# Kernel tuning notes

Hardware: AMD Instinct MI355X
Metric: run time of the kernel (lower is better)

## Reference

```python
import jax, jax.numpy as jnp
import numpy as np

B, T, C = 4, 2048, 1024
N_HEAD = 16
D_HEAD = C // N_HEAD


def setup_inputs() -> dict:
    key = jax.random.key(0)
    ks = jax.random.split(key, 5)
    s_in = 1.0 / np.sqrt(C)
    return {
        "x": jax.random.normal(ks[0], (B, T, C), dtype=jnp.float32),
        "Wqkv": jax.random.uniform(ks[1], (C, 3 * C), dtype=jnp.float32, minval=-s_in, maxval=s_in),
        "bqkv": jax.random.uniform(ks[2], (3 * C,), dtype=jnp.float32, minval=-s_in, maxval=s_in),
        "Wproj": jax.random.uniform(ks[3], (C, C), dtype=jnp.float32, minval=-s_in, maxval=s_in),
        "bproj": jax.random.uniform(ks[4], (C,), dtype=jnp.float32, minval=-s_in, maxval=s_in),
    }


def reference(x, Wqkv, bqkv, Wproj, bproj):
    b, t, c = x.shape
    qkv = x @ Wqkv + bqkv                      # [B,T,3C]
    q, k, v = jnp.split(qkv, 3, axis=2)
    # [B,T,H,Dh] -> [B,H,T,Dh]
    q = q.reshape(b, t, N_HEAD, D_HEAD).transpose(0, 2, 1, 3)
    k = k.reshape(b, t, N_HEAD, D_HEAD).transpose(0, 2, 1, 3)
    v = v.reshape(b, t, N_HEAD, D_HEAD).transpose(0, 2, 1, 3)
    scale = 1.0 / np.sqrt(D_HEAD).astype(np.float32)
    att = jnp.einsum("bhqd,bhkd->bhqk", q, k) * scale   # [B,H,T,T]
    causal = jnp.tril(jnp.ones((t, t), dtype=bool))
    att = jnp.where(causal, att, jnp.float32(-jnp.inf))
    att = jax.nn.softmax(att, axis=-1)
    y = jnp.einsum("bhqk,bhkd->bhqd", att, v)            # [B,H,T,Dh]
    y = y.transpose(0, 2, 1, 3).reshape(b, t, c)
    return y @ Wproj + bproj
```

## Files before the change

kernel.cpp:

```cpp
#include <hip/hip_runtime.h>

using u16 = unsigned short;
typedef __attribute__((ext_vector_type(8))) __bf16 bf16x8;
typedef __attribute__((ext_vector_type(4))) float f32x4;
typedef __attribute__((ext_vector_type(16))) float f32x16;
typedef __attribute__((ext_vector_type(4))) unsigned int u32x4;
typedef __attribute__((ext_vector_type(2))) unsigned int u32x2;

__device__ inline u16 f2bf(float f) {
    unsigned u = __float_as_uint(f);
    u += 0x7FFFu + ((u >> 16) & 1u);
    return (u16)(u >> 16);
}
__device__ inline unsigned pack2(float a, float b) {
    return (unsigned)f2bf(a) | ((unsigned)f2bf(b) << 16);
}
__device__ inline bf16x8 as_bf16x8(u32x4 v) {
    union { u32x4 u; bf16x8 b; } x; x.u = v; return x.b;
}
__device__ inline unsigned cvtpk(float lo, float hi) {
    unsigned w;
    asm("v_cvt_pk_bf16_f32 %0, %1, %2" : "=v"(w) : "v"(lo), "v"(hi));
    return w;
}
__device__ inline void gload_lds16(const void* g, void* l) {
    __builtin_amdgcn_global_load_lds(
        (const __attribute__((address_space(1))) void*)g,
        (__attribute__((address_space(3))) void*)l, 16, 0, 0);
}
__device__ inline void ring_barrier() {
    __builtin_amdgcn_sched_barrier(0);
    asm volatile("s_waitcnt lgkmcnt(0)" ::: "memory");
    __builtin_amdgcn_sched_barrier(0);
    __builtin_amdgcn_s_barrier();
    __builtin_amdgcn_sched_barrier(0);
}

__global__ __launch_bounds__(256) void xcast(const float* __restrict__ in,
                                             u16* __restrict__ out) {
    const size_t i = ((size_t)blockIdx.x * 256 + threadIdx.x) * 8;
    f32x4 a = *(const f32x4*)(in + i);
    f32x4 b = *(const f32x4*)(in + i + 4);
    u32x4 w;
    w[0] = pack2(a[0], a[1]); w[1] = pack2(a[2], a[3]);
    w[2] = pack2(b[0], b[1]); w[3] = pack2(b[2], b[3]);
    *(u32x4*)(out + i) = w;
}

__global__ __launch_bounds__(256) void tcast2(const float* __restrict__ Wqkv,
                                              const float* __restrict__ Wproj,
                                              u16* __restrict__ Wtq,
                                              u16* __restrict__ Wtp) {
    __shared__ float tile[64][65];
    const int by = blockIdx.y;
    const float* in;
    u16* out;
    int C, c0;
    if (by < 48) { in = Wqkv;  out = Wtq; C = 3072; c0 = by * 64; }
    else         { in = Wproj; out = Wtp; C = 1024; c0 = (by - 48) * 64; }
    const int R = 1024, r0 = blockIdx.x * 64;
    const int t = threadIdx.x;
    {
        const int r = t >> 2, cq = (t & 3) * 16;
        const float* src = in + (size_t)(r0 + r) * C + c0 + cq;
#pragma unroll
        for (int j = 0; j < 4; ++j) {
            f32x4 v = *(const f32x4*)(src + j * 4);
#pragma unroll
            for (int e = 0; e < 4; ++e) tile[r][cq + j * 4 + e] = v[e];
        }
    }
    __syncthreads();
    {
        const int c = t >> 2, rq = (t & 3) * 16;
        u32x4 w0, w1;
#pragma unroll
        for (int j = 0; j < 4; ++j) {
            w0[j] = pack2(tile[rq + 2 * j][c], tile[rq + 2 * j + 1][c]);
            w1[j] = pack2(tile[rq + 8 + 2 * j][c], tile[rq + 8 + 2 * j + 1][c]);
        }
        u16* dst = out + (size_t)(c0 + c) * R + r0 + rq;
        *(u32x4*)dst = w0;
        *(u32x4*)(dst + 8) = w1;
    }
}

template <int EPI>
__global__ __launch_bounds__(256) void gemm_kernel(const u16* __restrict__ A,
                                                   const u16* __restrict__ Bt,
                                                   const float* __restrict__ bias,
                                                   void* __restrict__ outp,
                                                   u16* __restrict__ vtp,
                                                   const int M, const int N, const int K) {
    __shared__ char lds[49152];
    const int t = threadIdx.x;
    const int l = t & 63, wid = t >> 6;
    const int wr = wid >> 1, wc = wid & 1;
    const int g = l >> 4, lr = l & 15;
    const int m0 = blockIdx.x * 128, n0 = blockIdx.y * 128;

    f32x4 acc[4][4];
#pragma unroll
    for (int i = 0; i < 4; ++i)
#pragma unroll
        for (int j = 0; j < 4; ++j)
#pragma unroll
            for (int e = 0; e < 4; ++e) acc[i][j][e] = 0.f;

    const size_t Kb2 = (size_t)K * 2;
    const size_t rowbA = (size_t)(m0 + wid * 16 + (l >> 2)) * Kb2 + (l & 3) * 16;
    const size_t rowbB = (size_t)(n0 + wid * 16 + (l >> 2)) * Kb2 + (l & 3) * 16;
    const int kn = K >> 5;

    auto STAGE = [&](int kk) {
        char* buf = lds + (kk % 3) * 16384;
        const size_t kb = (size_t)kk * 64;
#pragma unroll
        for (int j = 0; j < 2; ++j) {
            gload_lds16((const char*)A + rowbA + j * 64 * Kb2 + kb,
                        buf + j * 4096 + wid * 1024);
            gload_lds16((const char*)Bt + rowbB + j * 64 * Kb2 + kb,
                        buf + 8192 + j * 4096 + wid * 1024);
        }
    };

    STAGE(0); STAGE(1);
#pragma unroll 1
    for (int kk = 0; kk < kn; ++kk) {
        if (kk + 1 < kn) asm volatile("s_waitcnt vmcnt(4)" ::: "memory");
        else             asm volatile("s_waitcnt vmcnt(0)" ::: "memory");
        ring_barrier();
        if (kk + 2 < kn) STAGE(kk + 2);
        const char* As = lds + (kk % 3) * 16384;
        const char* Bs = As + 8192;
        bf16x8 a[4], b[4];
#pragma unroll
        for (int m = 0; m < 4; ++m) {
            const int row = wr * 64 + m * 16 + lr;
            a[m] = as_bf16x8(*(const u32x4*)(As + row * 64 + g * 16));
        }
#pragma unroll
        for (int n = 0; n < 4; ++n) {
            const int row = wc * 64 + n * 16 + lr;
            b[n] = as_bf16x8(*(const u32x4*)(Bs + row * 64 + g * 16));
        }
        __builtin_amdgcn_s_setprio(1);
#pragma unroll
        for (int m = 0; m < 4; ++m)
#pragma unroll
            for (int n = 0; n < 4; ++n)
                acc[m][n] = __builtin_amdgcn_mfma_f32_16x16x32_bf16(a[m], b[n], acc[m][n], 0, 0, 0);
        __builtin_amdgcn_s_setprio(0);
    }

    const float qsc = (EPI == 0 && n0 < 1024) ? 0.18033688f : 1.0f;
#pragma unroll
    for (int m = 0; m < 4; ++m) {
#pragma unroll
        for (int n = 0; n < 4; ++n) {
            const int colg = n0 + wc * 64 + n * 16 + lr;
            const float bv = bias[colg];
            if constexpr (EPI == 0) {
                const int sec = colg >> 10, c = colg & 1023;
                const int hh = c >> 6, dd = c & 63;
                if (sec == 2) {
                    const int rowg0 = m0 + wr * 64 + m * 16 + g * 4;
                    const int bb = rowg0 >> 11, tt = rowg0 & 2047;
                    u16 pk[4];
#pragma unroll
                    for (int r = 0; r < 4; ++r)
                        pk[r] = f2bf(acc[m][n][r] + bv);
                    u16* dst = vtp + (((size_t)(bb * 16 + hh) * 64 + dd) << 11) + tt;
                    unsigned w0 = (unsigned)pk[0] | ((unsigned)pk[1] << 16);
                    unsigned w1 = (unsigned)pk[2] | ((unsigned)pk[3] << 16);
                    u32x2 wv; wv[0] = w0; wv[1] = w1;
                    *(u32x2*)dst = wv;
                } else {
#pragma unroll
                    for (int r = 0; r < 4; ++r) {
                        const int rowg = m0 + wr * 64 + m * 16 + g * 4 + r;
                        const float v = (acc[m][n][r] + bv) * qsc;
                        const int bb = rowg >> 11, tt = rowg & 2047;
                        u16* dst = (u16*)outp;
                        dst[(size_t)sec * 8388608u +
                            (((size_t)(bb * 16 + hh) * 2048 + tt) << 6) + dd] = f2bf(v);
                    }
                }
            } else {
#pragma unroll
                for (int r = 0; r < 4; ++r) {
                    const int rowg = m0 + wr * 64 + m * 16 + g * 4 + r;
                    ((float*)outp)[(size_t)rowg * N + colg] = acc[m][n][r] + bv;
                }
            }
        }
    }
}

__global__ __launch_bounds__(256) void attn_kernel(const u16* __restrict__ Q,
                                                   const u16* __restrict__ K,
                                                   const u16* __restrict__ Vt,
                                                   u16* __restrict__ Y) {
    __shared__ char lds[32768];
    const int t = threadIdx.x;
    const int l = t & 63, w = t >> 6;
    const int q = l & 31, hi = l >> 5;
    const int id = (int)blockIdx.y * 16 + (int)blockIdx.x;
    const int p = 15 - (id >> 6);
    const int bh = id & 63;
    const char* Kby = (const char*)(K + (size_t)bh * 131072);
    const char* Vby = (const char*)(Vt + (size_t)bh * 131072);
    const u16* Qb = Q + (size_t)bh * 131072;
    const int bb = bh >> 4, hh = bh & 15;
    const unsigned ck = (unsigned)(((l & 7) ^ (l >> 3)) << 4);
    const unsigned rd_swz = (unsigned)((q & 7) << 4);

    const int q0w = p * 128 + w * 32;
    const int qg = q0w + q;
    const int NT = 2 * p + 2;
    const int ntw = ((q0w + 31) >> 6) + 1;

    bf16x8 qf[4];
#pragma unroll
    for (int ks = 0; ks < 4; ++ks)
        qf[ks] = as_bf16x8(*(const u32x4*)(Qb + (size_t)(q0w + q) * 64 + ks * 16 + hi * 8));

    f32x16 o0, o1;
#pragma unroll
    for (int r = 0; r < 16; ++r) { o0[r] = 0.f; o1[r] = 0.f; }
    float lacc = 0.f;

    auto STAGE = [&](int it) {
        const int kv0 = it << 6;
        char* base = lds + (it & 1) * 16384;
#pragma unroll
        for (int j = 0; j < 2; ++j) {
            const int r = w * 16 + j * 8 + (l >> 3);
            gload_lds16(Kby + (size_t)(kv0 + r) * 128 + ck,
                        base + w * 2048 + j * 1024);
            gload_lds16(Vby + (size_t)r * 4096 + (size_t)kv0 * 2 + ck,
                        base + 8192 + w * 2048 + j * 1024);
        }
    };

    STAGE(0);
#pragma unroll 1
    for (int it = 0; it < NT; ++it) {
        asm volatile("s_waitcnt vmcnt(0)" ::: "memory");
        ring_barrier();
        if (it + 1 < NT) STAGE(it + 1);
        if (it < ntw) {
            const int kv0 = it << 6;
            const char* Kl = lds + (it & 1) * 16384;
            const char* Vl = Kl + 8192;
            u32x4 vf[8];
#pragma unroll
            for (int kvb = 0; kvb < 2; ++kvb)
#pragma unroll
                for (int s = 0; s < 2; ++s)
#pragma unroll
                    for (int db = 0; db < 2; ++db)
                        vf[kvb * 4 + s * 2 + db] = *(const u32x4*)(
                            Vl + (unsigned)((db * 32 + q) * 128) +
                            ((unsigned)(kvb * 64 + s * 32 + hi * 16) ^ rd_swz));
            f32x16 s0, s1;
#pragma unroll
            for (int r = 0; r < 16; ++r) { s0[r] = 0.f; s1[r] = 0.f; }
            __builtin_amdgcn_s_setprio(1);
#pragma unroll
            for (int ks = 0; ks < 4; ++ks) {
                const unsigned co = (unsigned)(ks * 32 + hi * 16) ^ rd_swz;
                bf16x8 kf0 = as_bf16x8(*(const u32x4*)(Kl + (unsigned)(q * 128) + co));
                s0 = __builtin_amdgcn_mfma_f32_32x32x16_bf16(kf0, qf[ks], s0, 0, 0, 0);
                bf16x8 kf1 = as_bf16x8(*(const u32x4*)(Kl + (unsigned)((32 + q) * 128) + co));
                s1 = __builtin_amdgcn_mfma_f32_32x32x16_bf16(kf1, qf[ks], s1, 0, 0, 0);
            }
            __builtin_amdgcn_s_setprio(0);
            if (kv0 + 63 > q0w) {
#pragma unroll
                for (int r = 0; r < 16; ++r) {
                    const int roff = (r & 3) + 8 * (r >> 2) + hi * 4;
                    if (kv0 + roff > qg) s0[r] = -1.0e30f;
                    if (kv0 + 32 + roff > qg) s1[r] = -1.0e30f;
                }
            }
            float sm[8];
#pragma unroll
            for (int j = 0; j < 8; ++j) {
                s0[2 * j]     = exp2f(s0[2 * j]);
                s0[2 * j + 1] = exp2f(s0[2 * j + 1]);
                s1[2 * j]     = exp2f(s1[2 * j]);
                s1[2 * j + 1] = exp2f(s1[2 * j + 1]);
                sm[j] = (s0[2 * j] + s0[2 * j + 1]) + (s1[2 * j] + s1[2 * j + 1]);
            }
            lacc += ((sm[0] + sm[1]) + (sm[2] + sm[3])) +
                    ((sm[4] + sm[5]) + (sm[6] + sm[7]));
#pragma unroll
            for (int kvb = 0; kvb < 2; ++kvb) {
                unsigned wd[8];
#pragma unroll
                for (int j = 0; j < 8; ++j) {
                    const float plo = kvb ? s1[2 * j] : s0[2 * j];
                    const float phi = kvb ? s1[2 * j + 1] : s0[2 * j + 1];
                    wd[j] = cvtpk(plo, phi);
                }
                u32x2 r0 = __builtin_amdgcn_permlane32_swap(wd[0], wd[2], false, false);
                u32x2 r1 = __builtin_amdgcn_permlane32_swap(wd[1], wd[3], false, false);
                u32x2 r2 = __builtin_amdgcn_permlane32_swap(wd[4], wd[6], false, false);
                u32x2 r3 = __builtin_amdgcn_permlane32_swap(wd[5], wd[7], false, false);
                u32x4 fa, fb;
                fa[0] = r0[0]; fa[1] = r1[0]; fa[2] = r0[1]; fa[3] = r1[1];
                fb[0] = r2[0]; fb[1] = r3[0]; fb[2] = r2[1]; fb[3] = r3[1];
                const bf16x8 pa = as_bf16x8(fa), pb = as_bf16x8(fb);
                __builtin_amdgcn_s_setprio(1);
                o0 = __builtin_amdgcn_mfma_f32_32x32x16_bf16(pa, as_bf16x8(vf[kvb * 4 + 0]), o0, 0, 0, 0);
                o1 = __builtin_amdgcn_mfma_f32_32x32x16_bf16(pa, as_bf16x8(vf[kvb * 4 + 1]), o1, 0, 0, 0);
                o0 = __builtin_amdgcn_mfma_f32_32x32x16_bf16(pb, as_bf16x8(vf[kvb * 4 + 2]), o0, 0, 0, 0);
                o1 = __builtin_amdgcn_mfma_f32_32x32x16_bf16(pb, as_bf16x8(vf[kvb * 4 + 3]), o1, 0, 0, 0);
                __builtin_amdgcn_s_setprio(0);
            }
        }
    }
    float lsum;
    {
        u32x2 rr = __builtin_amdgcn_permlane32_swap(
            __float_as_uint(lacc), __float_as_uint(lacc), false, false);
        lsum = lacc + __uint_as_float(hi ? rr[0] : rr[1]);
    }
    const float linv = 1.f / lsum;
#pragma unroll
    for (int r = 0; r < 16; ++r) {
        const int roff = (r & 3) + 8 * (r >> 2) + hi * 4;
        const float invq = __shfl(linv, roff);
        const size_t base = ((size_t)(bb * 2048 + q0w + roff)) * 1024 + hh * 64 + q;
        Y[base] = f2bf(o0[r] * invq);
        Y[base + 32] = f2bf(o1[r] * invq);
    }
}

extern "C" void kernel_launch(void* const* d_in, const int* in_sizes, int n_in,
                              void* d_out, int out_size, void* d_ws, size_t ws_size,
                              hipStream_t stream) {
    const float* x = (const float*)d_in[0];
    const float* Wqkv = (const float*)d_in[1];
    const float* bqkv = (const float*)d_in[2];
    const float* Wproj = (const float*)d_in[3];
    const float* bproj = (const float*)d_in[4];
    float* out = (float*)d_out;
    char* ws = (char*)d_ws;

    u16* Wtq = (u16*)(ws + 0);
    u16* Wtp = (u16*)(ws + 6291456);
    u16* Qb  = (u16*)(ws + 8388608);
    u16* Yb  = (u16*)(ws + 41943040);
    u16* Vtb = (u16*)(ws + 58720256);
    u16* Xb  = (u16*)(ws + 75497472);

    xcast<<<4096, 256, 0, stream>>>(x, Xb);
    tcast2<<<dim3(16, 64), 256, 0, stream>>>(Wqkv, Wproj, Wtq, Wtp);
    gemm_kernel<0><<<dim3(64, 24), 256, 0, stream>>>(
        Xb, Wtq, bqkv, (void*)Qb, Vtb, 8192, 3072, 1024);
    attn_kernel<<<dim3(16, 64), 256, 0, stream>>>(
        Qb, Qb + 8388608, Vtb, Yb);
    gemm_kernel<1><<<dim3(64, 8), 256, 0, stream>>>(
        Yb, Wtp, bproj, (void*)out, nullptr, 8192, 1024, 1024);
}
```

Baseline: 182.9 us.

## Split longest causal attention query blocks across two workgroups and merge partials

```diff
diff --git a/kernel.cpp b/kernel.cpp
--- a/kernel.cpp
+++ b/kernel.cpp
@@ -197,17 +197,28 @@
     }
 }
 
+static const unsigned char TPj[20] = {11,10, 9, 7,15,15, 8,14,13,13,12,14, 5, 4,12, 6, 0, 2, 1, 3};
+static const unsigned char TCj[20] = { 0, 0, 0, 0, 0, 1, 0, 0, 0, 1, 0, 1, 0, 0, 1, 0, 0, 0, 0, 0};
+static const unsigned char TSj[20] = { 0, 0, 0, 0, 1, 1, 0, 1, 1, 1, 1, 1, 0, 0, 1, 0, 0, 0, 0, 0};
+
 __global__ __launch_bounds__(256) void attn_kernel(const u16* __restrict__ Q,
                                                    const u16* __restrict__ K,
                                                    const u16* __restrict__ Vt,
-                                                   u16* __restrict__ Y) {
+                                                   u16* __restrict__ Y,
+                                                   float* __restrict__ PartO,
+                                                   float* __restrict__ PartL) {
     __shared__ char lds[32768];
     const int t = threadIdx.x;
     const int l = t & 63, w = t >> 6;
     const int q = l & 31, hi = l >> 5;
-    const int id = (int)blockIdx.y * 16 + (int)blockIdx.x;
-    const int p = 15 - (id >> 6);
-    const int bh = id & 63;
+    const int bh = (int)blockIdx.x;
+    const int j = (int)blockIdx.y;
+    const int p  = (int)TPj[j];
+    const int cc = (int)TCj[j];
+    const int sp = (int)TSj[j];
+    const int half = p + 1;
+    const int t0  = (sp && cc) ? half : 0;
+    const int NTc = sp ? half : (2 * p + 2);
     const char* Kby = (const char*)(K + (size_t)bh * 131072);
     const char* Vby = (const char*)(Vt + (size_t)bh * 131072);
     const u16* Qb = Q + (size_t)bh * 131072;
@@ -217,7 +228,6 @@
 
     const int q0w = p * 128 + w * 32;
     const int qg = q0w + q;
-    const int NT = 2 * p + 2;
     const int ntw = ((q0w + 31) >> 6) + 1;
 
     bf16x8 qf[4];
@@ -230,28 +240,29 @@
     for (int r = 0; r < 16; ++r) { o0[r] = 0.f; o1[r] = 0.f; }
     float lacc = 0.f;
 
-    auto STAGE = [&](int it) {
-        const int kv0 = it << 6;
-        char* base = lds + (it & 1) * 16384;
-#pragma unroll
-        for (int j = 0; j < 2; ++j) {
-            const int r = w * 16 + j * 8 + (l >> 3);
+    auto STAGE = [&](int itl) {
+        const int kv0 = (t0 + itl) << 6;
+        char* base = lds + (itl & 1) * 16384;
+#pragma unroll
+        for (int jj = 0; jj < 2; ++jj) {
+            const int r = w * 16 + jj * 8 + (l >> 3);
             gload_lds16(Kby + (size_t)(kv0 + r) * 128 + ck,
-                        base + w * 2048 + j * 1024);
+                        base + w * 2048 + jj * 1024);
             gload_lds16(Vby + (size_t)r * 4096 + (size_t)kv0 * 2 + ck,
-                        base + 8192 + w * 2048 + j * 1024);
+                        base + 8192 + w * 2048 + jj * 1024);
         }
     };
 
     STAGE(0);
 #pragma unroll 1
-    for (int it = 0; it < NT; ++it) {
+    for (int itl = 0; itl < NTc; ++itl) {
         asm volatile("s_waitcnt vmcnt(0)" ::: "memory");
         ring_barrier();
-        if (it + 1 < NT) STAGE(it + 1);
-        if (it < ntw) {
-            const int kv0 = it << 6;
-            const char* Kl = lds + (it & 1) * 16384;
+        if (itl + 1 < NTc) STAGE(itl + 1);
+        const int tile = t0 + itl;
+        if (tile < ntw) {
+            const int kv0 = tile << 6;
+            const char* Kl = lds + (itl & 1) * 16384;
             const char* Vl = Kl + 8192;
             u32x4 vf[8];
 #pragma unroll
@@ -286,12 +297,12 @@
             }
             float sm[8];
 #pragma unroll
-            for (int j = 0; j < 8; ++j) {
-                s0[2 * j]     = exp2f(s0[2 * j]);
-                s0[2 * j + 1] = exp2f(s0[2 * j + 1]);
-                s1[2 * j]     = exp2f(s1[2 * j]);
-                s1[2 * j + 1] = exp2f(s1[2 * j + 1]);
-                sm[j] = (s0[2 * j] + s0[2 * j + 1]) + (s1[2 * j] + s1[2 * j + 1]);
+            for (int jj = 0; jj < 8; ++jj) {
+                s0[2 * jj]     = exp2f(s0[2 * jj]);
+                s0[2 * jj + 1] = exp2f(s0[2 * jj + 1]);
+                s1[2 * jj]     = exp2f(s1[2 * jj]);
+                s1[2 * jj + 1] = exp2f(s1[2 * jj + 1]);
+                sm[jj] = (s0[2 * jj] + s0[2 * jj + 1]) + (s1[2 * jj] + s1[2 * jj + 1]);
             }
             lacc += ((sm[0] + sm[1]) + (sm[2] + sm[3])) +
                     ((sm[4] + sm[5]) + (sm[6] + sm[7]));
@@ -299,10 +310,10 @@
             for (int kvb = 0; kvb < 2; ++kvb) {
                 unsigned wd[8];
 #pragma unroll
-                for (int j = 0; j < 8; ++j) {
-                    const float plo = kvb ? s1[2 * j] : s0[2 * j];
-                    const float phi = kvb ? s1[2 * j + 1] : s0[2 * j + 1];
-                    wd[j] = cvtpk(plo, phi);
+                for (int jj = 0; jj < 8; ++jj) {
+                    const float plo = kvb ? s1[2 * jj] : s0[2 * jj];
+                    const float phi = kvb ? s1[2 * jj + 1] : s0[2 * jj + 1];
+                    wd[jj] = cvtpk(plo, phi);
                 }
                 u32x2 r0 = __builtin_amdgcn_permlane32_swap(wd[0], wd[2], false, false);
                 u32x2 r1 = __builtin_amdgcn_permlane32_swap(wd[1], wd[3], false, false);
@@ -327,14 +338,57 @@
             __float_as_uint(lacc), __float_as_uint(lacc), false, false);
         lsum = lacc + __uint_as_float(hi ? rr[0] : rr[1]);
     }
-    const float linv = 1.f / lsum;
-#pragma unroll
-    for (int r = 0; r < 16; ++r) {
-        const int roff = (r & 3) + 8 * (r >> 2) + hi * 4;
-        const float invq = __shfl(linv, roff);
-        const size_t base = ((size_t)(bb * 2048 + q0w + roff)) * 1024 + hh * 64 + q;
-        Y[base] = f2bf(o0[r] * invq);
-        Y[base + 32] = f2bf(o1[r] * invq);
+    if (!sp) {
+        const float linv = 1.f / lsum;
+#pragma unroll
+        for (int r = 0; r < 16; ++r) {
+            const int roff = (r & 3) + 8 * (r >> 2) + hi * 4;
+            const float invq = __shfl(linv, roff);
+            const size_t base = ((size_t)(bb * 2048 + q0w + roff)) * 1024 + hh * 64 + q;
+            Y[base] = f2bf(o0[r] * invq);
+            Y[base + 32] = f2bf(o1[r] * invq);
+        }
+    } else {
+        const int sIdx = p - 12;
+        float* po = PartO + ((size_t)((sIdx * 2 + cc) * 64 + bh)) * 8192;
+#pragma unroll
+        for (int r = 0; r < 16; ++r) {
+            const int roff = (r & 3) + 8 * (r >> 2) + hi * 4;
+            const int row = w * 32 + roff;
+            po[row * 64 + q] = o0[r];
+            po[row * 64 + 32 + q] = o1[r];
+        }
+        if (l < 32)
+            PartL[((sIdx * 2 + cc) * 64 + bh) * 128 + w * 32 + q] = lsum;
+    }
+}
+
+__global__ __launch_bounds__(256) void attn_merge(const float* __restrict__ PO,
+                                                  const float* __restrict__ PL,
+                                                  u16* __restrict__ Y) {
+    const int bh = blockIdx.x, s = blockIdx.y;
+    const int t = threadIdx.x;
+    const int row = t >> 1, d0 = (t & 1) * 32;
+    const size_t pa = ((size_t)((s * 2 + 0) * 64 + bh)) * 8192 + row * 64 + d0;
+    const size_t pb = ((size_t)((s * 2 + 1) * 64 + bh)) * 8192 + row * 64 + d0;
+    const float la = PL[((s * 2 + 0) * 64 + bh) * 128 + row];
+    const float lb = PL[((s * 2 + 1) * 64 + bh) * 128 + row];
+    const float inv = 1.f / (la + lb);
+    const int bb = bh >> 4, hh = bh & 15;
+    const int trow = 1536 + s * 128 + row;
+    u16* dst = Y + ((size_t)(bb * 2048 + trow)) * 1024 + hh * 64 + d0;
+#pragma unroll
+    for (int blk = 0; blk < 4; ++blk) {
+        f32x4 a0 = *(const f32x4*)(PO + pa + blk * 8);
+        f32x4 a1 = *(const f32x4*)(PO + pa + blk * 8 + 4);
+        f32x4 b0 = *(const f32x4*)(PO + pb + blk * 8);
+        f32x4 b1 = *(const f32x4*)(PO + pb + blk * 8 + 4);
+        u32x4 wv;
+        wv[0] = pack2((a0[0] + b0[0]) * inv, (a0[1] + b0[1]) * inv);
+        wv[1] = pack2((a0[2] + b0[2]) * inv, (a0[3] + b0[3]) * inv);
+        wv[2] = pack2((a1[0] + b1[0]) * inv, (a1[1] + b1[1]) * inv);
+        wv[3] = pack2((a1[2] + b1[2]) * inv, (a1[3] + b1[3]) * inv);
+        *(u32x4*)(dst + blk * 8) = wv;
     }
 }
 
@@ -355,13 +409,16 @@
     u16* Yb  = (u16*)(ws + 41943040);
     u16* Vtb = (u16*)(ws + 58720256);
     u16* Xb  = (u16*)(ws + 75497472);
+    float* PartO = (float*)(ws + 75497472);
+    float* PartL = (float*)(ws + 0);
 
     xcast<<<4096, 256, 0, stream>>>(x, Xb);
     tcast2<<<dim3(16, 64), 256, 0, stream>>>(Wqkv, Wproj, Wtq, Wtp);
     gemm_kernel<0><<<dim3(64, 24), 256, 0, stream>>>(
         Xb, Wtq, bqkv, (void*)Qb, Vtb, 8192, 3072, 1024);
-    attn_kernel<<<dim3(16, 64), 256, 0, stream>>>(
-        Qb, Qb + 8388608, Vtb, Yb);
+    attn_kernel<<<dim3(64, 20), 256, 0, stream>>>(
+        Qb, Qb + 8388608, Vtb, Yb, PartO, PartL);
+    attn_merge<<<dim3(64, 4), 256, 0, stream>>>(PartO, PartL, Yb);
     gemm_kernel<1><<<dim3(64, 8), 256, 0, stream>>>(
         Yb, Wtp, bproj, (void*)out, nullptr, 8192, 1024, 1024);
 }
```

Result: slower. 188.3 us (+3.0%).
